# Optimization experiments

Hardware: AMD Instinct MI355X
Metric: run time of the kernel (lower is better)

The kernel has to match this reference:

```python
import jax, jax.numpy as jnp
import numpy as np

K = 7        # kernel_size
STRIDE = 1
PAD = 3
DIL = 1
N, C, H, W = 8, 64, 56, 56

def setup_inputs() -> dict:
    key = jax.random.key(0)
    k1, k2 = jax.random.split(key)
    input1 = jax.random.normal(k1, (N, C, H, W), dtype=jnp.float32)
    input2 = jax.random.normal(k2, (N, C, H, W), dtype=jnp.float32)
    return {"input1": input1, "input2": input2}

def _subtraction2_refpad(x1, x2):
    n, c, h, w = x1.shape
    eff = DIL * (K - 1) + 1
    h_out = (h + 2 * PAD - eff) // STRIDE + 1
    w_out = (w + 2 * PAD - eff) // STRIDE + 1
    # center offset into unpadded input1: h_in_center = -PAD + h*STRIDE + (K-1)//2*DIL
    ch = -PAD + (K - 1) // 2 * DIL  # = 0 for K=7,PAD=3,DIL=1
    cw = ch
    x1c = x1[:, :, ch:ch + (h_out - 1) * STRIDE + 1:STRIDE,
                   cw:cw + (w_out - 1) * STRIDE + 1:STRIDE]  # [n,c,h_out,w_out]
    # reflect-pad input2 (matches CUDA reflect index math: h_in<0 -> -h_in, etc.)
    x2p = jnp.pad(x2, ((0, 0), (0, 0), (PAD, PAD), (PAD, PAD)), mode='reflect')
    windows = []
    for kh in range(K):
        for kw in range(K):
            hs = kh * DIL
            ws = kw * DIL
            windows.append(
                x2p[:, :, hs:hs + (h_out - 1) * STRIDE + 1:STRIDE,
                          ws:ws + (w_out - 1) * STRIDE + 1:STRIDE])
    win = jnp.stack(windows, axis=2)  # [n, c, K*K, h_out, w_out]
    out = x1c[:, :, None, :, :] - win
    return out.reshape(n, c * K * K, h_out, w_out)

def reference(input1, input2):
    return _subtraction2_refpad(input1, input2)
```

## Files before the change

### kernel.cpp

```cpp
#include <hip/hip_runtime.h>


typedef float f4 __attribute__((ext_vector_type(4)));

constexpr int N_   = 8;
constexpr int C_   = 64;
constexpr int H_   = 56;
constexpr int W_   = 56;
constexpr int K_   = 7;
constexpr int PAD_ = 3;
constexpr int W4_  = W_ / 4;
constexpr int TPC_ = K_ * H_ * W4_;
constexpr int HW_  = H_ * W_;

__device__ __forceinline__ int refl(int i) {
    i = (i < 0) ? -i : i;
    return (i < H_) ? i : (2 * (H_ - 1) - i);
}

__global__ __launch_bounds__(256)
void sub2_kernel(const float* __restrict__ x1,
                 const float* __restrict__ x2,
                 float* __restrict__ out)
{
    int t = blockIdx.x * 256 + threadIdx.x;
    if (t >= TPC_) return;

    int w4 = t % W4_;
    int r  = t / W4_;
    int h  = r % H_;
    int kh = r / H_;

    int nc = blockIdx.y;
    int hs = refl(h + kh - PAD_);

    const float* __restrict__ x1row = x1 + ((size_t)nc * H_ + h) * W_;
    const float* __restrict__ x2row = x2 + ((size_t)nc * H_ + hs) * W_;

    int w0 = w4 * 4;
    f4 a = *reinterpret_cast<const f4*>(x1row + w0);

    int wb = w0 - 4;
    wb = wb < 0 ? 0 : (wb > 44 ? 44 : wb);
    f4 f0 = *reinterpret_cast<const f4*>(x2row + wb);
    f4 f1 = *reinterpret_cast<const f4*>(x2row + wb + 4);
    f4 f2 = *reinterpret_cast<const f4*>(x2row + wb + 8);
    float f[12] = {f0.x, f0.y, f0.z, f0.w, f1.x, f1.y, f1.z, f1.w,
                   f2.x, f2.y, f2.z, f2.w};

    bool eL = (w4 == 0);
    bool eR = (w4 == W4_ - 1);

    constexpr int pL[10] = {3, 2, 1, 0, 1, 2, 3, 4, 5, 6};
    constexpr int pR[10] = {5, 6, 7, 8, 9, 10, 11, 10, 9, 8};
    float b[10];
#pragma unroll
    for (int j = 0; j < 10; ++j)
        b[j] = eL ? f[pL[j]] : (eR ? f[pR[j]] : f[j + 1]);

    float* __restrict__ obase =
        out + (((size_t)nc * (K_ * K_) + kh * K_) * H_ + h) * W_ + w0;

#pragma unroll
    for (int kw = 0; kw < K_; ++kw) {
        f4 v;
        v.x = a.x - b[kw + 0];
        v.y = a.y - b[kw + 1];
        v.z = a.z - b[kw + 2];
        v.w = a.w - b[kw + 3];
        __builtin_nontemporal_store(v, reinterpret_cast<f4*>(obase + (size_t)kw * HW_));
    }
}

extern "C" void kernel_launch(void* const* d_in, const int* in_sizes, int n_in,
                              void* d_out, int out_size, void* d_ws, size_t ws_size,
                              hipStream_t stream) {
    const float* x1 = (const float*)d_in[0];
    const float* x2 = (const float*)d_in[1];
    float* out = (float*)d_out;

    dim3 grid((TPC_ + 255) / 256, N_ * C_);
    sub2_kernel<<<grid, 256, 0, stream>>>(x1, x2, out);
}
```

Baseline: 62.13 us.

## Stage each channel plane in LDS and loop over output sites per block

Each block now handles one (n,c) plane. It copies that plane of both inputs into shared memory (about 25 KB), then loops over all K*H*W/4 output sites, reading the window values from LDS rather than global memory. The aim is to cut redundant global and L2 reads of input2 and input1, which were previously re-fetched by every kh row and neighbouring thread. In exchange the grid drops to 512 blocks of 512 threads, and each block waits at a barrier before storing, which reduces parallelism and memory-level overlap in a kernel that is dominated by output writes.

```diff
diff --git a/kernel.cpp b/kernel.cpp
--- a/kernel.cpp
+++ b/kernel.cpp
@@ -3,72 +3,88 @@
 
 typedef float f4 __attribute__((ext_vector_type(4)));
 
-constexpr int N_   = 8;
-constexpr int C_   = 64;
-constexpr int H_   = 56;
-constexpr int W_   = 56;
-constexpr int K_   = 7;
-constexpr int PAD_ = 3;
-constexpr int W4_  = W_ / 4;
-constexpr int TPC_ = K_ * H_ * W4_;
-constexpr int HW_  = H_ * W_;
+constexpr int N_    = 8;
+constexpr int C_    = 64;
+constexpr int H_    = 56;
+constexpr int W_    = 56;
+constexpr int K_    = 7;
+constexpr int PAD_  = 3;
+constexpr int W4_   = W_ / 4;
+constexpr int HW_   = H_ * W_;
+constexpr int PLANE4_ = HW_ / 4;
+constexpr int SITES_  = K_ * H_ * W4_;
+constexpr int TPB_  = 512;
 
 __device__ __forceinline__ int refl(int i) {
     i = (i < 0) ? -i : i;
     return (i < H_) ? i : (2 * (H_ - 1) - i);
 }
 
-__global__ __launch_bounds__(256)
+__global__ __launch_bounds__(TPB_)
 void sub2_kernel(const float* __restrict__ x1,
                  const float* __restrict__ x2,
                  float* __restrict__ out)
 {
-    int t = blockIdx.x * 256 + threadIdx.x;
-    if (t >= TPC_) return;
+    __shared__ float lds1[HW_];
+    __shared__ float lds2[HW_];
 
-    int w4 = t % W4_;
-    int r  = t / W4_;
-    int h  = r % H_;
-    int kh = r / H_;
+    int nc  = blockIdx.x;
+    int tid = threadIdx.x;
 
-    int nc = blockIdx.y;
-    int hs = refl(h + kh - PAD_);
+    const float* __restrict__ p1 = x1 + (size_t)nc * HW_;
+    const float* __restrict__ p2 = x2 + (size_t)nc * HW_;
 
-    const float* __restrict__ x1row = x1 + ((size_t)nc * H_ + h) * W_;
-    const float* __restrict__ x2row = x2 + ((size_t)nc * H_ + hs) * W_;
+#pragma unroll
+    for (int i = tid; i < PLANE4_; i += TPB_) {
+        reinterpret_cast<f4*>(lds1)[i] = reinterpret_cast<const f4*>(p1)[i];
+        reinterpret_cast<f4*>(lds2)[i] = reinterpret_cast<const f4*>(p2)[i];
+    }
+    __syncthreads();
 
-    int w0 = w4 * 4;
-    f4 a = *reinterpret_cast<const f4*>(x1row + w0);
-
-    int wb = w0 - 4;
-    wb = wb < 0 ? 0 : (wb > 44 ? 44 : wb);
-    f4 f0 = *reinterpret_cast<const f4*>(x2row + wb);
-    f4 f1 = *reinterpret_cast<const f4*>(x2row + wb + 4);
-    f4 f2 = *reinterpret_cast<const f4*>(x2row + wb + 8);
-    float f[12] = {f0.x, f0.y, f0.z, f0.w, f1.x, f1.y, f1.z, f1.w,
-                   f2.x, f2.y, f2.z, f2.w};
-
-    bool eL = (w4 == 0);
-    bool eR = (w4 == W4_ - 1);
+    float* __restrict__ oplane = out + (size_t)nc * (K_ * K_) * HW_;
 
     constexpr int pL[10] = {3, 2, 1, 0, 1, 2, 3, 4, 5, 6};
     constexpr int pR[10] = {5, 6, 7, 8, 9, 10, 11, 10, 9, 8};
-    float b[10];
+
+    for (int s = tid; s < SITES_; s += TPB_) {
+        int w4 = s % W4_;
+        int r  = s / W4_;
+        int h  = r % H_;
+        int kh = r / H_;
+
+        int hs = refl(h + kh - PAD_);
+        int w0 = w4 * 4;
+
+        f4 a = *reinterpret_cast<const f4*>(lds1 + h * W_ + w0);
+
+        int wb = w0 - 4;
+        wb = wb < 0 ? 0 : (wb > 44 ? 44 : wb);
+        const float* xr = lds2 + hs * W_ + wb;
+        f4 f0 = *reinterpret_cast<const f4*>(xr);
+        f4 f1 = *reinterpret_cast<const f4*>(xr + 4);
+        f4 f2 = *reinterpret_cast<const f4*>(xr + 8);
+        float f[12] = {f0.x, f0.y, f0.z, f0.w, f1.x, f1.y, f1.z, f1.w,
+                       f2.x, f2.y, f2.z, f2.w};
+
+        bool eL = (w4 == 0);
+        bool eR = (w4 == W4_ - 1);
+
+        float b[10];
 #pragma unroll
-    for (int j = 0; j < 10; ++j)
-        b[j] = eL ? f[pL[j]] : (eR ? f[pR[j]] : f[j + 1]);
+        for (int j = 0; j < 10; ++j)
+            b[j] = eL ? f[pL[j]] : (eR ? f[pR[j]] : f[j + 1]);
 
-    float* __restrict__ obase =
-        out + (((size_t)nc * (K_ * K_) + kh * K_) * H_ + h) * W_ + w0;
+        float* obase = oplane + (size_t)(kh * K_) * HW_ + h * W_ + w0;
 
 #pragma unroll
-    for (int kw = 0; kw < K_; ++kw) {
-        f4 v;
-        v.x = a.x - b[kw + 0];
-        v.y = a.y - b[kw + 1];
-        v.z = a.z - b[kw + 2];
-        v.w = a.w - b[kw + 3];
-        __builtin_nontemporal_store(v, reinterpret_cast<f4*>(obase + (size_t)kw * HW_));
+        for (int kw = 0; kw < K_; ++kw) {
+            f4 v;
+            v.x = a.x - b[kw + 0];
+            v.y = a.y - b[kw + 1];
+            v.z = a.z - b[kw + 2];
+            v.w = a.w - b[kw + 3];
+            __builtin_nontemporal_store(v, reinterpret_cast<f4*>(obase + (size_t)kw * HW_));
+        }
     }
 }
 
@@ -79,6 +95,5 @@
     const float* x2 = (const float*)d_in[1];
     float* out = (float*)d_out;
 
-    dim3 grid((TPC_ + 255) / 256, N_ * C_);
-    sub2_kernel<<<grid, 256, 0, stream>>>(x1, x2, out);
+    sub2_kernel<<<dim3(N_ * C_), TPB_, 0, stream>>>(x1, x2, out);
 }
```

After: 68.70 us. +10.6%, slower.
